# Optimization experiments

Hardware: AMD Instinct MI355X
Metric: run time of the kernel (lower is better)

## Reference

```python
import jax, jax.numpy as jnp
import numpy as np

T, N, F = 8, 384, 32
N_TYPE, MAX_NODE, IN_DIM, HID = 3, 130, 256, 64  # IN_DIM = T*F
C = IN_DIM // 2  # graph channels = conv channels = 128 = MAX_NODE - 2


def setup_inputs():
    key = jax.random.key(0)
    ks = jax.random.split(key, 10)
    V = jax.random.normal(ks[0], (1, T, N, F + 1), dtype=jnp.float32)
    types = (jnp.arange(N) % N_TYPE + 1).astype(jnp.float32)  # exactly 128 nodes per type
    V = V.at[..., -1].set(types)
    graph = jax.random.normal(ks[1], (C, N, N), dtype=jnp.float32)
    u = lambda k, s: jax.random.uniform(k, s, jnp.float32, -0.1, 0.1)
    return dict(
        V=V,
        graph=graph,
        node_type=(jnp.arange(N) % N_TYPE + 1).astype(jnp.int32),
        ex=1,
        lin0_w=u(ks[2], (MAX_NODE // 2, MAX_NODE)),
        lin0_b=u(ks[3], (MAX_NODE // 2,)),
        att_lin_w=u(ks[4], (N_TYPE, HID, IN_DIM)),
        att_lin_b=u(ks[5], (N_TYPE, HID)),
        agg=jax.random.uniform(ks[6], (N_TYPE, 2 * HID, 1), jnp.float32, -1.0, 1.0),
        pl=u(ks[7], (1,)),
        conv2_w=u(ks[8], (C, C, 2, 2)),
        conv2_b=u(ks[9], (C,)),
    )


def _forward(V, graph, lin0_w, lin0_b, att_lin_w, att_lin_b, agg, pl, conv2_w, conv2_b):
    Vs = V[0]                                   # [T, N, F+1]
    t_vec = Vs[0, :, -1].astype(jnp.int32)      # [N], node types in 1..n_type
    feats = jnp.transpose(Vs[:, :, :-1], (1, 0, 2)).reshape(N, T * F)  # [N, T*F]

    # per-type stable gather + zero-pad to MAX_NODE, then node-dim Linear(max_node -> max_node//2)
    def per_type(k):
        mask = t_vec == (k + 1)
        idx = jnp.argsort(jnp.logical_not(mask), stable=True)[:MAX_NODE]
        vk = feats[idx] * mask[idx][:, None].astype(feats.dtype)   # [MAX_NODE, D]
        vk = (vk.T @ lin0_w.T + lin0_b).T                          # [MAX_NODE//2, D]
        return vk

    v = jax.vmap(per_type)(jnp.arange(N_TYPE))  # [n_type, M2, D]

    # TypeAttentionLayer per type idx: linear -> concat with row idx -> agg matmul -> lrelu -> max over nodes -> softmax over types
    def att_layer(Wk, bk, aggk, k):
        x = jnp.einsum('tnd,hd->tnh', v, Wk) + bk               # [n_type, M2, H]
        xi = jnp.take(x, k, axis=0)                             # [M2, H]
        x2 = jnp.concatenate([x, jnp.broadcast_to(xi, x.shape)], axis=-1)  # [n_type, M2, 2H]
        s = jax.nn.leaky_relu(jnp.einsum('tnh,h->tn', x2, aggk[:, 0]))     # slope 0.01, as torch
        return jax.nn.softmax(jnp.max(s, axis=1), axis=0)       # [n_type]

    A = jax.vmap(att_layer)(att_lin_w, att_lin_b, agg, jnp.arange(N_TYPE))  # [n_type, n_type]

    # scatter per-type-pair scores into adjacency: att_mx[i,j] = A[t_i-1, t_j-1]
    att_mx = A[t_vec[:, None] - 1, t_vec[None, :] - 1]          # [N, N]
    wei = graph * att_mx                                        # ablation == 0

    # nb_cnn: zero-pad bottom/right by MAX_NODE - len(graph) = MAX_NODE - C, then valid 2x2 convs back to NxN
    pad = MAX_NODE - C
    wg = jnp.pad(wei, ((0, 0), (0, pad), (0, pad)))
    for _ in range(pad):
        wg = jax.lax.conv_general_dilated(
            wg[None], conv2_w, (1, 1), 'VALID',
            dimension_numbers=('NCHW', 'OIHW', 'NCHW'))[0] + conv2_b[:, None, None]

    out = pl * wg + graph                                       # univ == 2
    return jax.nn.relu(out)                                     # sparse


def reference(V, graph, node_type, ex, lin0_w, lin0_b, att_lin_w, att_lin_b, agg, pl, conv2_w, conv2_b):
    if not ex:
        return None
    return _forward(V, graph, lin0_w, lin0_b, att_lin_w, att_lin_b, agg, pl, conv2_w, conv2_b)
```

## Files before the change

### kernel.cpp

```cpp
#include <hip/hip_runtime.h>

typedef __attribute__((ext_vector_type(8))) short bf16x8;
typedef __attribute__((ext_vector_type(4))) float f32x4;
typedef unsigned int u32;
typedef unsigned short u16;
typedef unsigned long long u64;

#define S0 384
#define PLANE0 (384 * 384)
#define XR 386
#define XROWB ((size_t)XR * 256)

#define GLOAD_LDS(g, l) __builtin_amdgcn_global_load_lds( \
    (const __attribute__((address_space(1))) void*)(g),   \
    (__attribute__((address_space(3))) void*)(l), 16, 0, 0)

__device__ __forceinline__ u16 bfr(float f) {
    u32 b = __float_as_uint(f);
    b += 0x7fff + ((b >> 16) & 1);
    return (u16)(b >> 16);
}

__global__ void k_v(const float* __restrict__ V,
                    const float* __restrict__ lin0_w,
                    const float* __restrict__ lin0_b,
                    float* __restrict__ v_out) {
    int blk = blockIdx.x;
    int k = blk / 65, m = blk % 65;
    int d = threadIdx.x;
    int t = d >> 5, f = d & 31;
    const float* vbase = V + (size_t)t * 384 * 33 + f;
    float acc = lin0_b[m];
    for (int r = 0; r < 128; ++r) {
        float w = lin0_w[m * 130 + r];
        acc += w * vbase[(3 * r + k) * 33];
    }
    v_out[(size_t)blk * 256 + d] = acc;
}

__global__ void k_att(const float* __restrict__ v,
                      const float* __restrict__ att_w,
                      const float* __restrict__ att_b,
                      const float* __restrict__ agg,
                      float* __restrict__ A_out) {
    int k = blockIdx.x;
    int tid = threadIdx.x;
    __shared__ float wv1[256], wv2[256];
    __shared__ float sbuf[3][65];
    __shared__ float Ck_s;
    __shared__ float sm[3];
    {
        int d = tid;
        float a1 = 0.f, a2 = 0.f;
        for (int h = 0; h < 64; ++h) {
            float w = att_w[((size_t)(k * 64 + h)) * 256 + d];
            a1 += agg[k * 128 + h] * w;
            a2 += agg[k * 128 + 64 + h] * w;
        }
        wv1[d] = a1;
        wv2[d] = a2;
    }
    if (tid == 0) {
        float c = 0.f;
        for (int h = 0; h < 64; ++h)
            c += (agg[k * 128 + h] + agg[k * 128 + 64 + h]) * att_b[k * 64 + h];
        Ck_s = c;
    }
    __syncthreads();
    if (tid < 195) {
        int t = tid / 65, m = tid % 65;
        const float* vt = v + ((size_t)(t * 65 + m)) * 256;
        const float* vk = v + ((size_t)(k * 65 + m)) * 256;
        float s = Ck_s;
        for (int d = 0; d < 256; ++d)
            s += vt[d] * wv1[d] + vk[d] * wv2[d];
        s = s > 0.f ? s : 0.01f * s;
        sbuf[t][m] = s;
    }
    __syncthreads();
    if (tid < 3) {
        float mx = sbuf[tid][0];
        for (int m = 1; m < 65; ++m) mx = fmaxf(mx, sbuf[tid][m]);
        sm[tid] = mx;
    }
    __syncthreads();
    if (tid == 0) {
        float mx = fmaxf(sm[0], fmaxf(sm[1], sm[2]));
        float e0 = __expf(sm[0] - mx), e1 = __expf(sm[1] - mx), e2 = __expf(sm[2] - mx);
        float inv = 1.f / (e0 + e1 + e2);
        A_out[k * 3 + 0] = e0 * inv;
        A_out[k * 3 + 1] = e1 * inv;
        A_out[k * 3 + 2] = e2 * inv;
    }
}

__global__ void k_prep_E(const float* __restrict__ cw, const float* __restrict__ cb,
                         u16* __restrict__ Ebf2, float* __restrict__ beff) {
    int o = blockIdx.x, i = threadIdx.x;
    __shared__ float4 Wo[128];
    __shared__ float red[128];
    Wo[i] = *(const float4*)(cw + (size_t)(o * 128 + i) * 4);
    __syncthreads();
    float a9[9];
#pragma unroll
    for (int q = 0; q < 9; ++q) a9[q] = 0.f;
    for (int m = 0; m < 128; ++m) {
        float4 w1 = *(const float4*)(cw + (size_t)(m * 128 + i) * 4);
        float4 w2 = Wo[m];
        a9[0] += w2.x * w1.x;
        a9[1] += w2.x * w1.y + w2.y * w1.x;
        a9[2] += w2.y * w1.y;
        a9[3] += w2.x * w1.z + w2.z * w1.x;
        a9[4] += w2.x * w1.w + w2.y * w1.z + w2.z * w1.y + w2.w * w1.x;
        a9[5] += w2.y * w1.w + w2.w * w1.y;
        a9[6] += w2.z * w1.z;
        a9[7] += w2.z * w1.w + w2.w * w1.z;
        a9[8] += w2.w * w1.w;
    }
    int icg = i >> 5, el = i & 31;
#pragma unroll
    for (int q = 0; q < 9; ++q)
        Ebf2[(size_t)((q * 4 + icg) * 128 + o) * 32 + el] = bfr(a9[q]);
    float4 wo = Wo[i];
    red[i] = cb[i] * (wo.x + wo.y + wo.z + wo.w);
    __syncthreads();
    for (int s = 64; s > 0; s >>= 1) {
        if (i < s) red[i] += red[i + s];
        __syncthreads();
    }
    if (i == 0) beff[o] = cb[o] + red[0];
}

__global__ __launch_bounds__(256) void k_pack(
        const float* __restrict__ graph,
        const float* __restrict__ A9g,
        u16* __restrict__ X) {
    __shared__ u16 T[128 * 136];
    const int tid = threadIdx.x;
    const int xt = blockIdx.x, y = blockIdx.y;
    const int x0p = xt * 128;
    const uint4 z = {0u, 0u, 0u, 0u};

    if (y >= 384) {
        int nunits = (xt == 2) ? 130 * 16 : 128 * 16;
        for (int u = tid; u < nunits; u += 256) {
            int x = x0p + (u >> 4), j = u & 15;
            *(uint4*)((char*)X + ((size_t)y * XR + x) * 256 + j * 16) = z;
        }
        return;
    }

    const int ic0 = (tid & 31) * 4;
    const int xc = tid >> 5;
    float ar[3];
    ar[0] = A9g[(y % 3) * 3 + 0];
    ar[1] = A9g[(y % 3) * 3 + 1];
    ar[2] = A9g[(y % 3) * 3 + 2];
    const int m0 = (x0p + xc * 16) % 3;
    float facs[3];
    facs[0] = ar[m0];
    facs[1] = ar[m0 + 1 == 3 ? 0 : m0 + 1];
    facs[2] = ar[m0 + 2 >= 3 ? m0 - 1 : m0 + 2];

    float vals[4][16];
#pragma unroll
    for (int ici = 0; ici < 4; ++ici) {
        const float* g = graph + (size_t)(ic0 + ici) * PLANE0 + (size_t)y * S0 + x0p + xc * 16;
#pragma unroll
        for (int q = 0; q < 4; ++q) {
            float4 f = *(const float4*)(g + q * 4);
            vals[ici][q * 4 + 0] = f.x;
            vals[ici][q * 4 + 1] = f.y;
            vals[ici][q * 4 + 2] = f.z;
            vals[ici][q * 4 + 3] = f.w;
        }
    }
#pragma unroll
    for (int e = 0; e < 16; ++e) {
        float f = facs[e % 3];
        int x = xc * 16 + e;
        u16 q0 = bfr(vals[0][e] * f);
        u16 q1 = bfr(vals[1][e] * f);
        u16 q2 = bfr(vals[2][e] * f);
        u16 q3 = bfr(vals[3][e] * f);
        u64 w = (u64)q0 | ((u64)q1 << 16) | ((u64)q2 << 32) | ((u64)q3 << 48);
        *(u64*)(T + x * 136 + ic0) = w;
    }
    __syncthreads();

#pragma unroll
    for (int i = 0; i < 8; ++i) {
        int u = tid + 256 * i;
        int x = u >> 4, j = u & 15;
        int oct = j ^ (x & 15);
        uint4 w = *(const uint4*)(T + x * 136 + oct * 8);
        *(uint4*)((char*)X + ((size_t)y * XR + x0p + x) * 256 + j * 16) = w;
    }
    if (xt == 2 && tid < 32) {
        int x = 384 + (tid >> 4), j = tid & 15;
        *(uint4*)((char*)X + ((size_t)y * XR + x) * 256 + j * 16) = z;
    }
}

__global__ __launch_bounds__(256, 2) void k_conv9(
        const u16* __restrict__ X,
        const short* __restrict__ Ebf2,
        const float* __restrict__ beff,
        const float* __restrict__ pl,
        const float* __restrict__ graph,
        float* __restrict__ out) {
    __shared__ __align__(16) char Bt[67584];
    const int tid = threadIdx.x;
    const int lane = tid & 63, wave = tid >> 6;
    const int l15 = lane & 15, l16 = lane >> 4;

    const int phys = blockIdx.x;
    const int logical = (phys & 7) * 144 + (phys >> 3);
    const int bx = logical % 6, by = logical / 6;
    const int x0 = bx * 64, y0 = by * 2;
    const int mh = wave & 1, rh = wave >> 1;
    const int ocbase = mh * 64;

    {
        const char* gsrc = (const char*)X + ((size_t)y0 * XR + x0) * 256;
#pragma unroll
        for (int r = 0; r < 4; ++r) {
            const char* rs = gsrc + (size_t)r * XROWB;
            char* ld = Bt + r * 16896;
#pragma unroll
            for (int i = 0; i < 4; ++i)
                GLOAD_LDS(rs + (size_t)tid * 16 + i * 4096, ld + tid * 16 + i * 4096);
            if (tid < 32)
                GLOAD_LDS(rs + (size_t)tid * 16 + 16384, ld + tid * 16 + 16384);
        }
    }

#define ALOAD(dst, s) {                                                        \
        const short* Ap = Ebf2 + ((size_t)((s) * 128 + ocbase + l15) << 5)     \
                          + l16 * 8;                                           \
        dst[0] = *(const bf16x8*)(Ap);                                         \
        dst[1] = *(const bf16x8*)(Ap + 512);                                   \
        dst[2] = *(const bf16x8*)(Ap + 1024);                                  \
        dst[3] = *(const bf16x8*)(Ap + 1536); }

    bf16x8 ap[4][4];
    ALOAD(ap[0], 0); ALOAD(ap[1], 1); ALOAD(ap[2], 2); ALOAD(ap[3], 3);

    __syncthreads();

    f32x4 acc[4][4];
#pragma unroll
    for (int a = 0; a < 4; ++a)
#pragma unroll
        for (int b = 0; b < 4; ++b)
            acc[a][b] = (f32x4){0.f, 0.f, 0.f, 0.f};

#define BADDR(s, n) (Bt + (rh + ((s) >> 2) / 3) * 16896                        \
        + ((l15 + (n) * 16 + ((s) >> 2) % 3) << 8)                             \
        + (((((s) & 3) * 4 + l16) ^ ((l15 + (n) * 16 + ((s) >> 2) % 3) & 15)) << 4))

    bf16x8 bp[2][4];
#pragma unroll
    for (int n = 0; n < 4; ++n) bp[0][n] = *(const bf16x8*)BADDR(0, n);

#pragma unroll
    for (int s = 0; s < 36; ++s) {
        const int cur = s & 1;
        if (s < 35) {
#pragma unroll
            for (int n = 0; n < 4; ++n)
                bp[cur ^ 1][n] = *(const bf16x8*)BADDR(s + 1, n);
        }
        __builtin_amdgcn_s_setprio(1);
#pragma unroll
        for (int n = 0; n < 4; ++n) {
            acc[0][n] = __builtin_amdgcn_mfma_f32_16x16x32_bf16(ap[s & 3][0], bp[cur][n], acc[0][n], 0, 0, 0);
            acc[1][n] = __builtin_amdgcn_mfma_f32_16x16x32_bf16(ap[s & 3][1], bp[cur][n], acc[1][n], 0, 0, 0);
            acc[2][n] = __builtin_amdgcn_mfma_f32_16x16x32_bf16(ap[s & 3][2], bp[cur][n], acc[2][n], 0, 0, 0);
            acc[3][n] = __builtin_amdgcn_mfma_f32_16x16x32_bf16(ap[s & 3][3], bp[cur][n], acc[3][n], 0, 0, 0);
        }
        __builtin_amdgcn_s_setprio(0);
        if (s + 4 < 36) ALOAD(ap[s & 3], s + 4);
    }
#undef ALOAD
#undef BADDR

    const float plv = pl[0];
    const int yy = y0 + rh;
#pragma unroll
    for (int m = 0; m < 4; ++m) {
#pragma unroll
        for (int r4 = 0; r4 < 4; ++r4) {
            const int oc = ocbase + m * 16 + l16 * 4 + r4;
            const float bias = beff[oc];
            const float* grow = graph + (size_t)oc * PLANE0 + (size_t)yy * S0 + x0;
            float* orow = out + (size_t)oc * PLANE0 + (size_t)yy * S0 + x0;
#pragma unroll
            for (int n = 0; n < 4; ++n) {
                const int xx = n * 16 + l15;
                float v = plv * (acc[m][n][r4] + bias) + grow[xx];
                orow[xx] = v > 0.f ? v : 0.f;
            }
        }
    }
}

extern "C" void kernel_launch(void* const* d_in, const int* in_sizes, int n_in,
                              void* d_out, int out_size, void* d_ws, size_t ws_size,
                              hipStream_t stream) {
    (void)in_sizes; (void)n_in; (void)out_size; (void)ws_size;
    const float* V      = (const float*)d_in[0];
    const float* graph  = (const float*)d_in[1];
    const float* lin0_w = (const float*)d_in[4];
    const float* lin0_b = (const float*)d_in[5];
    const float* att_w  = (const float*)d_in[6];
    const float* att_b  = (const float*)d_in[7];
    const float* agg    = (const float*)d_in[8];
    const float* pl     = (const float*)d_in[9];
    const float* cw     = (const float*)d_in[10];
    const float* cb     = (const float*)d_in[11];
    float* out = (float*)d_out;

    char* ws = (char*)d_ws;
    float* v_ws  = (float*)ws;
    float* A_ws  = (float*)(ws + 200704);
    u16*   Ebf2  = (u16*)(ws + 200768);
    float* beff  = (float*)(ws + 495680);
    u16*   X     = (u16*)(ws + 496192);

    k_prep_E<<<128, 128, 0, stream>>>(cw, cb, Ebf2, beff);
    k_v<<<195, 256, 0, stream>>>(V, lin0_w, lin0_b, v_ws);
    k_att<<<3, 256, 0, stream>>>(v_ws, att_w, att_b, agg, A_ws);
    k_pack<<<dim3(3, 386), 256, 0, stream>>>(graph, A_ws, X);
    k_conv9<<<1152, 256, 0, stream>>>(
        X, (const short*)Ebf2, beff, pl, graph, out);
}
```

Measured before the change: 140.9 us.

## Load conv B operands directly from global memory and merge prep kernels

```diff
diff --git a/kernel.cpp b/kernel.cpp
--- a/kernel.cpp
+++ b/kernel.cpp
@@ -11,31 +11,66 @@
 #define XR 386
 #define XROWB ((size_t)XR * 256)
 
-#define GLOAD_LDS(g, l) __builtin_amdgcn_global_load_lds( \
-    (const __attribute__((address_space(1))) void*)(g),   \
-    (__attribute__((address_space(3))) void*)(l), 16, 0, 0)
-
 __device__ __forceinline__ u16 bfr(float f) {
     u32 b = __float_as_uint(f);
     b += 0x7fff + ((b >> 16) & 1);
     return (u16)(b >> 16);
 }
 
-__global__ void k_v(const float* __restrict__ V,
-                    const float* __restrict__ lin0_w,
-                    const float* __restrict__ lin0_b,
-                    float* __restrict__ v_out) {
-    int blk = blockIdx.x;
-    int k = blk / 65, m = blk % 65;
-    int d = threadIdx.x;
-    int t = d >> 5, f = d & 31;
-    const float* vbase = V + (size_t)t * 384 * 33 + f;
-    float acc = lin0_b[m];
-    for (int r = 0; r < 128; ++r) {
-        float w = lin0_w[m * 130 + r];
-        acc += w * vbase[(3 * r + k) * 33];
-    }
-    v_out[(size_t)blk * 256 + d] = acc;
+__global__ __launch_bounds__(256) void k_prep_v(
+        const float* __restrict__ cw, const float* __restrict__ cb,
+        u16* __restrict__ Ebf2, float* __restrict__ beff,
+        const float* __restrict__ V,
+        const float* __restrict__ lin0_w, const float* __restrict__ lin0_b,
+        float* __restrict__ v_out) {
+    const int tid = threadIdx.x;
+    if (blockIdx.x < 128) {
+        int o = blockIdx.x, i = tid & 127;
+        __shared__ float4 Wo[128];
+        __shared__ float red[128];
+        Wo[i] = *(const float4*)(cw + (size_t)(o * 128 + i) * 4);
+        __syncthreads();
+        float a9[9];
+#pragma unroll
+        for (int q = 0; q < 9; ++q) a9[q] = 0.f;
+        for (int m = 0; m < 128; ++m) {
+            float4 w1 = *(const float4*)(cw + (size_t)(m * 128 + i) * 4);
+            float4 w2 = Wo[m];
+            a9[0] += w2.x * w1.x;
+            a9[1] += w2.x * w1.y + w2.y * w1.x;
+            a9[2] += w2.y * w1.y;
+            a9[3] += w2.x * w1.z + w2.z * w1.x;
+            a9[4] += w2.x * w1.w + w2.y * w1.z + w2.z * w1.y + w2.w * w1.x;
+            a9[5] += w2.y * w1.w + w2.w * w1.y;
+            a9[6] += w2.z * w1.z;
+            a9[7] += w2.z * w1.w + w2.w * w1.z;
+            a9[8] += w2.w * w1.w;
+        }
+        int icg = i >> 5, el = i & 31;
+#pragma unroll
+        for (int q = 0; q < 9; ++q)
+            Ebf2[(size_t)((q * 4 + icg) * 128 + o) * 32 + el] = bfr(a9[q]);
+        float4 wo = Wo[i];
+        red[i] = cb[i] * (wo.x + wo.y + wo.z + wo.w);
+        __syncthreads();
+        for (int s = 64; s > 0; s >>= 1) {
+            if (tid < 128 && i < s) red[i] += red[i + s];
+            __syncthreads();
+        }
+        if (tid == 0) beff[o] = cb[o] + red[0];
+    } else {
+        int blk = blockIdx.x - 128;
+        int k = blk / 65, m = blk % 65;
+        int d = tid;
+        int t = d >> 5, f = d & 31;
+        const float* vbase = V + (size_t)t * 384 * 33 + f;
+        float acc = lin0_b[m];
+        for (int r = 0; r < 128; ++r) {
+            float w = lin0_w[m * 130 + r];
+            acc += w * vbase[(3 * r + k) * 33];
+        }
+        v_out[(size_t)blk * 256 + d] = acc;
+    }
 }
 
 __global__ void k_att(const float* __restrict__ v,
@@ -94,43 +129,6 @@
     }
 }
 
-__global__ void k_prep_E(const float* __restrict__ cw, const float* __restrict__ cb,
-                         u16* __restrict__ Ebf2, float* __restrict__ beff) {
-    int o = blockIdx.x, i = threadIdx.x;
-    __shared__ float4 Wo[128];
-    __shared__ float red[128];
-    Wo[i] = *(const float4*)(cw + (size_t)(o * 128 + i) * 4);
-    __syncthreads();
-    float a9[9];
-#pragma unroll
-    for (int q = 0; q < 9; ++q) a9[q] = 0.f;
-    for (int m = 0; m < 128; ++m) {
-        float4 w1 = *(const float4*)(cw + (size_t)(m * 128 + i) * 4);
-        float4 w2 = Wo[m];
-        a9[0] += w2.x * w1.x;
-        a9[1] += w2.x * w1.y + w2.y * w1.x;
-        a9[2] += w2.y * w1.y;
-        a9[3] += w2.x * w1.z + w2.z * w1.x;
-        a9[4] += w2.x * w1.w + w2.y * w1.z + w2.z * w1.y + w2.w * w1.x;
-        a9[5] += w2.y * w1.w + w2.w * w1.y;
-        a9[6] += w2.z * w1.z;
-        a9[7] += w2.z * w1.w + w2.w * w1.z;
-        a9[8] += w2.w * w1.w;
-    }
-    int icg = i >> 5, el = i & 31;
-#pragma unroll
-    for (int q = 0; q < 9; ++q)
-        Ebf2[(size_t)((q * 4 + icg) * 128 + o) * 32 + el] = bfr(a9[q]);
-    float4 wo = Wo[i];
-    red[i] = cb[i] * (wo.x + wo.y + wo.z + wo.w);
-    __syncthreads();
-    for (int s = 64; s > 0; s >>= 1) {
-        if (i < s) red[i] += red[i + s];
-        __syncthreads();
-    }
-    if (i == 0) beff[o] = cb[o] + red[0];
-}
-
 __global__ __launch_bounds__(256) void k_pack(
         const float* __restrict__ graph,
         const float* __restrict__ A9g,
@@ -202,14 +200,13 @@
     }
 }
 
-__global__ __launch_bounds__(256, 2) void k_conv9(
+__global__ __launch_bounds__(256, 3) void k_conv9(
         const u16* __restrict__ X,
         const short* __restrict__ Ebf2,
         const float* __restrict__ beff,
         const float* __restrict__ pl,
         const float* __restrict__ graph,
         float* __restrict__ out) {
-    __shared__ __align__(16) char Bt[67584];
     const int tid = threadIdx.x;
     const int lane = tid & 63, wave = tid >> 6;
     const int l15 = lane & 15, l16 = lane >> 4;
@@ -221,19 +218,7 @@
     const int mh = wave & 1, rh = wave >> 1;
     const int ocbase = mh * 64;
 
-    {
-        const char* gsrc = (const char*)X + ((size_t)y0 * XR + x0) * 256;
-#pragma unroll
-        for (int r = 0; r < 4; ++r) {
-            const char* rs = gsrc + (size_t)r * XROWB;
-            char* ld = Bt + r * 16896;
-#pragma unroll
-            for (int i = 0; i < 4; ++i)
-                GLOAD_LDS(rs + (size_t)tid * 16 + i * 4096, ld + tid * 16 + i * 4096);
-            if (tid < 32)
-                GLOAD_LDS(rs + (size_t)tid * 16 + 16384, ld + tid * 16 + 16384);
-        }
-    }
+    const char* Xbase = (const char*)X + ((size_t)(y0 + rh) * XR + x0) * 256;
 
 #define ALOAD(dst, s) {                                                        \
         const short* Ap = Ebf2 + ((size_t)((s) * 128 + ocbase + l15) << 5)     \
@@ -243,10 +228,19 @@
         dst[2] = *(const bf16x8*)(Ap + 1024);                                  \
         dst[3] = *(const bf16x8*)(Ap + 1536); }
 
-    bf16x8 ap[4][4];
-    ALOAD(ap[0], 0); ALOAD(ap[1], 1); ALOAD(ap[2], 2); ALOAD(ap[3], 3);
-
-    __syncthreads();
+#define BOFF(s, n) ((size_t)(((s) >> 2) / 3) * XROWB                           \
+        + ((l15 + (n) * 16 + ((s) >> 2) % 3) << 8)                             \
+        + (((((s) & 3) * 4 + l16) ^ ((l15 + (n) * 16 + ((s) >> 2) % 3) & 15)) << 4))
+
+#define BLOAD(dst, s) {                                                        \
+        dst[0] = *(const bf16x8*)(Xbase + BOFF(s, 0));                         \
+        dst[1] = *(const bf16x8*)(Xbase + BOFF(s, 1));                         \
+        dst[2] = *(const bf16x8*)(Xbase + BOFF(s, 2));                         \
+        dst[3] = *(const bf16x8*)(Xbase + BOFF(s, 3)); }
+
+    bf16x8 ap[2][4], bp[2][4];
+    ALOAD(ap[0], 0); BLOAD(bp[0], 0);
+    ALOAD(ap[1], 1); BLOAD(bp[1], 1);
 
     f32x4 acc[4][4];
 #pragma unroll
@@ -255,35 +249,23 @@
         for (int b = 0; b < 4; ++b)
             acc[a][b] = (f32x4){0.f, 0.f, 0.f, 0.f};
 
-#define BADDR(s, n) (Bt + (rh + ((s) >> 2) / 3) * 16896                        \
-        + ((l15 + (n) * 16 + ((s) >> 2) % 3) << 8)                             \
-        + (((((s) & 3) * 4 + l16) ^ ((l15 + (n) * 16 + ((s) >> 2) % 3) & 15)) << 4))
-
-    bf16x8 bp[2][4];
-#pragma unroll
-    for (int n = 0; n < 4; ++n) bp[0][n] = *(const bf16x8*)BADDR(0, n);
-
 #pragma unroll
     for (int s = 0; s < 36; ++s) {
         const int cur = s & 1;
-        if (s < 35) {
-#pragma unroll
-            for (int n = 0; n < 4; ++n)
-                bp[cur ^ 1][n] = *(const bf16x8*)BADDR(s + 1, n);
-        }
         __builtin_amdgcn_s_setprio(1);
 #pragma unroll
         for (int n = 0; n < 4; ++n) {
-            acc[0][n] = __builtin_amdgcn_mfma_f32_16x16x32_bf16(ap[s & 3][0], bp[cur][n], acc[0][n], 0, 0, 0);
-            acc[1][n] = __builtin_amdgcn_mfma_f32_16x16x32_bf16(ap[s & 3][1], bp[cur][n], acc[1][n], 0, 0, 0);
-            acc[2][n] = __builtin_amdgcn_mfma_f32_16x16x32_bf16(ap[s & 3][2], bp[cur][n], acc[2][n], 0, 0, 0);
-            acc[3][n] = __builtin_amdgcn_mfma_f32_16x16x32_bf16(ap[s & 3][3], bp[cur][n], acc[3][n], 0, 0, 0);
+            acc[0][n] = __builtin_amdgcn_mfma_f32_16x16x32_bf16(ap[cur][0], bp[cur][n], acc[0][n], 0, 0, 0);
+            acc[1][n] = __builtin_amdgcn_mfma_f32_16x16x32_bf16(ap[cur][1], bp[cur][n], acc[1][n], 0, 0, 0);
+            acc[2][n] = __builtin_amdgcn_mfma_f32_16x16x32_bf16(ap[cur][2], bp[cur][n], acc[2][n], 0, 0, 0);
+            acc[3][n] = __builtin_amdgcn_mfma_f32_16x16x32_bf16(ap[cur][3], bp[cur][n], acc[3][n], 0, 0, 0);
         }
         __builtin_amdgcn_s_setprio(0);
-        if (s + 4 < 36) ALOAD(ap[s & 3], s + 4);
+        if (s + 2 < 36) { ALOAD(ap[cur], s + 2); BLOAD(bp[cur], s + 2); }
     }
 #undef ALOAD
-#undef BADDR
+#undef BLOAD
+#undef BOFF
 
     const float plv = pl[0];
     const int yy = y0 + rh;
@@ -328,8 +310,7 @@
     float* beff  = (float*)(ws + 495680);
     u16*   X     = (u16*)(ws + 496192);
 
-    k_prep_E<<<128, 128, 0, stream>>>(cw, cb, Ebf2, beff);
-    k_v<<<195, 256, 0, stream>>>(V, lin0_w, lin0_b, v_ws);
+    k_prep_v<<<323, 256, 0, stream>>>(cw, cb, Ebf2, beff, V, lin0_w, lin0_b, v_ws);
     k_att<<<3, 256, 0, stream>>>(v_ws, att_w, att_b, agg, A_ws);
     k_pack<<<dim3(3, 386), 256, 0, stream>>>(graph, A_ws, X);
     k_conv9<<<1152, 256, 0, stream>>>(
```

New measurement: 175.5 us. +24.6%, slower.
